# Kernel tuning notes

Measured on AMD Instinct MI355X. Metric: run time of the kernel, lower is better.

Reference implementation:

```python
import jax, jax.numpy as jnp
import numpy as np

B, CIN, T = 16, 1024, 2000
BN, OUT, K = 512, 512, 3
DIL = (1, 2, 3)
NBR = len(DIL)
RED = 1
BN_EPS = 1e-5
STD_EPS = 0.01


def setup_inputs() -> dict:
    key = jax.random.key(0)
    ks = jax.random.split(key, 16)
    inp = {
        "x": jax.random.normal(ks[0], (B, CIN, T), dtype=jnp.float32),
        # BatchNorm1d(in_channels) params + running stats (inference mode)
        "bn1_gamma": jax.random.uniform(ks[1], (CIN,), minval=0.5, maxval=1.5),
        "bn1_beta": jax.random.normal(ks[2], (CIN,)) * 0.1,
        "bn1_mean": jax.random.normal(ks[3], (CIN,)) * 0.1,
        "bn1_var": jax.random.uniform(ks[4], (CIN,), minval=0.5, maxval=1.5),
        # linear1: in_channels -> bn_channels, no bias
        "W1": jax.random.normal(ks[5], (BN, CIN)) * (1.0 / np.sqrt(CIN)),
        # BatchNorm1d(bn_channels)
        "bn2_gamma": jax.random.uniform(ks[6], (BN,), minval=0.5, maxval=1.5),
        "bn2_beta": jax.random.normal(ks[7], (BN,)) * 0.1,
        "bn2_mean": jax.random.normal(ks[8], (BN,)) * 0.1,
        "bn2_var": jax.random.uniform(ks[9], (BN,), minval=0.5, maxval=1.5),
        # per-dilation TimeDelay weights [n_branch, OUT, BN, K] (bias=False)
        "conv_w": jax.random.normal(ks[10], (NBR, OUT, BN, K)) * (1.0 / np.sqrt(OUT)),
        # StatsSelect: linear1 (4C -> C//red), linear2 list (C//red -> C)
        "sel_W1": jax.random.normal(ks[11], (OUT // RED, 4 * OUT)) * (1.0 / np.sqrt(4 * OUT)),
        "sel_b1": jax.random.normal(ks[12], (OUT // RED,)) * 0.01,
        "sel_W2": jax.random.normal(ks[13], (NBR, OUT, OUT // RED)) * (1.0 / np.sqrt(OUT // RED)),
        "sel_b2": jax.random.normal(ks[14], (NBR, OUT)) * 0.01,
    }
    return inp


def _bn_relu(x, gamma, beta, mean, var):
    # inference BatchNorm1d over channel dim, then ReLU; x: [B, C, T]
    inv = gamma / jnp.sqrt(var + BN_EPS)
    y = x * inv[None, :, None] + (beta - mean * inv)[None, :, None]
    return jax.nn.relu(y)


def _forward(x, bn1_gamma, bn1_beta, bn1_mean, bn1_var, W1,
             bn2_gamma, bn2_beta, bn2_mean, bn2_var,
             conv_w, sel_W1, sel_b1, sel_W2, sel_b2):
    # bn_function: nonlinear1 -> linear1 (pointwise over channels)
    h = _bn_relu(x, bn1_gamma, bn1_beta, bn1_mean, bn1_var)  # [B, CIN, T]
    h = jnp.einsum('bct,oc->bot', h, W1)                      # [B, BN, T]
    h = _bn_relu(h, bn2_gamma, bn2_beta, bn2_mean, bn2_var)
    # multi-dilation TDNN branches (dilated conv1d with 'same' padding)
    pad = (K - 1) // 2
    outs = []
    for i, d in enumerate(DIL):
        y = jax.lax.conv_general_dilated(
            h, conv_w[i], window_strides=(1,), padding=[(pad * d, pad * d)],
            rhs_dilation=(d,), dimension_numbers=('NCH', 'OIH', 'NCH'))
        outs.append(y)
    f = jnp.stack(outs, axis=1)  # [B, n, OUT, T]
    xs = jnp.sum(f, axis=1)      # [B, OUT, T]
    # high-order statistics pooling over time
    mean = jnp.mean(xs, axis=-1)                     # [B, OUT]
    std = jnp.std(xs, axis=-1, ddof=1)               # unbiased
    norm = (xs - mean[..., None]) / jnp.clip(std, STD_EPS)[..., None]
    skew = jnp.mean(norm ** 3, axis=-1)
    kurt = jnp.mean(norm ** 4, axis=-1)
    stats = jnp.concatenate([mean, std, skew, kurt], axis=-1)  # [B, 4*OUT]
    z = stats @ sel_W1.T + sel_b1                               # [B, OUT//RED]
    s = jnp.einsum('br,ncr->bnc', z, sel_W2) + sel_b2[None]     # [B, n, OUT]
    s = jax.nn.softmax(s, axis=1)[..., None]                    # [B, n, OUT, 1]
    return jnp.sum(f * s, axis=1)                               # [B, OUT, T]


def reference(x, bn1_gamma, bn1_beta, bn1_mean, bn1_var, W1,
              bn2_gamma, bn2_beta, bn2_mean, bn2_var,
              conv_w, sel_W1, sel_b1, sel_W2, sel_b2):
    return _forward(x, bn1_gamma, bn1_beta, bn1_mean, bn1_var, W1,
                    bn2_gamma, bn2_beta, bn2_mean, bn2_var,
                    conv_w, sel_W1, sel_b1, sel_W2, sel_b2)
```

## Files before the change

kernel.cpp:

```cpp
#include <hip/hip_runtime.h>
#include <hip/hip_bf16.h>

#define B_    16
#define CIN_  1024
#define T_    2000
#define BN_   512
#define OUT_  512
#define NBR_  3
#define TP_X  2048
#define TP_H  2064
#define HOFF  4

typedef float  f32x4  __attribute__((ext_vector_type(4)));
typedef __bf16 bf16x8 __attribute__((ext_vector_type(8)));
typedef unsigned short u16;
typedef u16 u16x4 __attribute__((ext_vector_type(4)));
typedef u16 u16x8 __attribute__((ext_vector_type(8)));

static __device__ __forceinline__ float b2f(u16 u) {
    union { float f; unsigned int i; } v; v.i = ((unsigned int)u) << 16; return v.f;
}
static __device__ __forceinline__ u16 f2b(float f) {
    __hip_bfloat16 h = __float2bfloat16(f);
    u16 r; __builtin_memcpy(&r, &h, 2); return r;
}
static __device__ __forceinline__ void gld16(const u16* g, u16* l) {
    __builtin_amdgcn_global_load_lds(
        (const __attribute__((address_space(1))) unsigned int*)g,
        (__attribute__((address_space(3))) unsigned int*)l, 16, 0, 0);
}

__global__ __launch_bounds__(256) void k_prep_x(
    const float* __restrict__ x, const float* __restrict__ g,
    const float* __restrict__ be, const float* __restrict__ mu,
    const float* __restrict__ va, u16* __restrict__ xbT)
{
    __shared__ float tile[32][33];
    int b = blockIdx.z, c0 = blockIdx.y * 32, t0 = blockIdx.x * 32;
    int tid = threadIdx.x;
    int cl = tid >> 3, tt = (tid & 7) * 4;
    int c = c0 + cl;
    float inv = g[c] / sqrtf(va[c] + 1e-5f);
    float bia = be[c] - mu[c] * inv;
    int t = t0 + tt;
    float y0 = 0.f, y1 = 0.f, y2 = 0.f, y3 = 0.f;
    if (t < T_) {
        float4 v = *reinterpret_cast<const float4*>(x + (size_t)(b * CIN_ + c) * T_ + t);
        y0 = fmaxf(v.x * inv + bia, 0.f);
        y1 = fmaxf(v.y * inv + bia, 0.f);
        y2 = fmaxf(v.z * inv + bia, 0.f);
        y3 = fmaxf(v.w * inv + bia, 0.f);
    }
    tile[tt + 0][cl] = y0; tile[tt + 1][cl] = y1;
    tile[tt + 2][cl] = y2; tile[tt + 3][cl] = y3;
    __syncthreads();
    int tl = tid >> 3, c8 = (tid & 7) * 4;
    u16x4 o;
    o.x = f2b(tile[tl][c8 + 0]);
    o.y = f2b(tile[tl][c8 + 1]);
    o.z = f2b(tile[tl][c8 + 2]);
    o.w = f2b(tile[tl][c8 + 3]);
    *reinterpret_cast<u16x4*>(xbT + (size_t)(b * TP_X + t0 + tl) * CIN_ + c0 + c8) = o;
}

__global__ __launch_bounds__(256) void k_prep_w1(
    const float* __restrict__ W1, const float* __restrict__ g,
    const float* __restrict__ be, const float* __restrict__ mu,
    const float* __restrict__ va, u16* __restrict__ W1b, float* __restrict__ bias2)
{
    int i = blockIdx.x * 256 + threadIdx.x;
    int o = i >> 8;
    int c = (i & 255) * 4;
    float inv = g[o] / sqrtf(va[o] + 1e-5f);
    if (c == 0) bias2[o] = be[o] - mu[o] * inv;
    float4 w = *reinterpret_cast<const float4*>(W1 + (size_t)o * CIN_ + c);
    u16x4 r;
    r.x = f2b(w.x * inv); r.y = f2b(w.y * inv);
    r.z = f2b(w.z * inv); r.w = f2b(w.w * inv);
    *reinterpret_cast<u16x4*>(W1b + (size_t)o * CIN_ + c) = r;
}

__global__ __launch_bounds__(256) void k_prep_wc(
    const float* __restrict__ cw, u16* __restrict__ wb)
{
    int i = blockIdx.x * 256 + threadIdx.x;
    if (i >= NBR_ * OUT_ * BN_) return;
    const float* p = cw + (size_t)i * 3;
    int c = i & 511;
    int o = (i >> 9) & 511;
    int n = i >> 18;
#pragma unroll
    for (int k = 0; k < 3; k++)
        wb[((size_t)(n * 3 + k) * OUT_ + o) * BN_ + c] = f2b(p[k]);
}

__global__ __launch_bounds__(256) void k_zero_hpad(u16* __restrict__ hT)
{
    int i = blockIdx.x * 256 + threadIdx.x;
    if (i >= B_ * 64 * BN_) return;
    int c = i & 511;
    int p = (i >> 9) % 64;
    int b = i / (64 * 512);
    int idx = (p < HOFF) ? p : (p + 2000);
    hT[(size_t)(b * TP_H + idx) * BN_ + c] = 0;
}

__global__ __launch_bounds__(256) void k_gemm1(
    const u16* __restrict__ W1b, const u16* __restrict__ xbT,
    const float* __restrict__ bias2, u16* __restrict__ hT)
{
    __shared__ u16 As[128 * 32];
    __shared__ u16 Bs[128 * 32];
    int tid = threadIdx.x;
    int t0 = blockIdx.x * 128;
    int o0 = blockIdx.y * 128;
    int b  = blockIdx.z;
    int lane = tid & 63, wv = tid >> 6;
    int m_off = (wv & 1) * 64, n_off = (wv >> 1) * 64;
    int lr = lane & 15, g = lane >> 4;

    int s0 = wv * 128 + lane, s1 = s0 + 64;
    size_t ga0 = (size_t)(s0 >> 2) * CIN_ + (((s0 & 3) ^ ((s0 >> 3) & 3)) * 8);
    size_t ga1 = (size_t)(s1 >> 2) * CIN_ + (((s1 & 3) ^ ((s1 >> 3) & 3)) * 8);
    u16* lA0 = As + (size_t)(wv * 128) * 8; u16* lA1 = lA0 + 512;
    u16* lB0 = Bs + (size_t)(wv * 128) * 8; u16* lB1 = lB0 + 512;

    int sw = (g ^ ((lr >> 1) & 3)) * 8;
    int fA[4], fB[4];
#pragma unroll
    for (int m = 0; m < 4; m++) fA[m] = (m_off + m * 16 + lr) * 32 + sw;
#pragma unroll
    for (int n = 0; n < 4; n++) fB[n] = (n_off + n * 16 + lr) * 32 + sw;

    f32x4 zz = {0.f, 0.f, 0.f, 0.f};
    f32x4 acc[4][4];
#pragma unroll
    for (int m = 0; m < 4; m++)
#pragma unroll
        for (int n = 0; n < 4; n++) acc[m][n] = zz;

    const u16* Ag = W1b + (size_t)o0 * CIN_;
    const u16* Bg = xbT + (size_t)(b * TP_X + t0) * CIN_;

    for (int kc = 0; kc < CIN_; kc += 32) {
        gld16(Ag + ga0 + kc, lA0);
        gld16(Ag + ga1 + kc, lA1);
        gld16(Bg + ga0 + kc, lB0);
        gld16(Bg + ga1 + kc, lB1);
        __syncthreads();
        bf16x8 af[4], bfr[4];
#pragma unroll
        for (int m = 0; m < 4; m++) af[m] = *reinterpret_cast<const bf16x8*>(As + fA[m]);
#pragma unroll
        for (int n = 0; n < 4; n++) bfr[n] = *reinterpret_cast<const bf16x8*>(Bs + fB[n]);
#pragma unroll
        for (int m = 0; m < 4; m++)
#pragma unroll
            for (int n = 0; n < 4; n++)
                acc[m][n] = __builtin_amdgcn_mfma_f32_16x16x32_bf16(af[m], bfr[n], acc[m][n], 0, 0, 0);
        __syncthreads();
    }

    int qr = (lane >> 4) * 4;
#pragma unroll
    for (int m = 0; m < 4; m++) {
        int o = o0 + m_off + m * 16 + qr;
        f32x4 bb = *reinterpret_cast<const f32x4*>(bias2 + o);
#pragma unroll
        for (int n = 0; n < 4; n++) {
            int t = t0 + n_off + n * 16 + lr;
            if (t < T_) {
                f32x4 v = acc[m][n];
                u16x4 r;
                r.x = f2b(fmaxf(v.x + bb.x, 0.f));
                r.y = f2b(fmaxf(v.y + bb.y, 0.f));
                r.z = f2b(fmaxf(v.z + bb.z, 0.f));
                r.w = f2b(fmaxf(v.w + bb.w, 0.f));
                *reinterpret_cast<u16x4*>(hT + (size_t)(b * TP_H + t + HOFF) * BN_ + o) = r;
            }
        }
    }
}

__global__ __launch_bounds__(256) void k_conv(
    const u16* __restrict__ hT, const u16* __restrict__ wb, u16* __restrict__ f)
{
    __shared__ u16 As[576 * 8];
    __shared__ u16 Bs[3 * 512 * 8];
    int tid = threadIdx.x;
    int t0 = blockIdx.x * 128;
    int o0 = blockIdx.y * 128;
    int nb = blockIdx.z;
    int n = nb >> 4, b = nb & 15;
    int d = n + 1;
    int lane = tid & 63, wv = tid >> 6;
    int m_off = (wv & 1) * 64, n_off = (wv >> 1) * 64;
    int lr = lane & 15, g = lane >> 4;

    int q1 = tid + 256;
    size_t off0 = (size_t)(tid >> 2) * BN_ + (((tid & 3) ^ ((tid >> 3) & 3)) * 8);
    size_t off1 = (size_t)(q1 >> 2) * BN_ + (((q1 & 3) ^ ((q1 >> 3) & 3)) * 8);
    int q2 = 512 + (lane & 31);
    size_t off2 = (size_t)(q2 >> 2) * BN_ + (((q2 & 3) ^ ((q2 >> 3) & 3)) * 8);
    u16* lA0 = As + (size_t)(wv * 64) * 8;
    u16* lA1 = As + (size_t)(256 + wv * 64) * 8;
    u16* lA2 = As + (size_t)512 * 8;
    u16* lB0 = Bs + (size_t)(wv * 64) * 8;
    u16* lB1 = Bs + (size_t)(256 + wv * 64) * 8;

    int sw = (g ^ ((lr >> 1) & 3)) * 8;
    int fB[4];
#pragma unroll
    for (int nn = 0; nn < 4; nn++) fB[nn] = (n_off + nn * 16 + lr) * 32 + sw;

    f32x4 zz = {0.f, 0.f, 0.f, 0.f};
    f32x4 acc[4][4];
#pragma unroll
    for (int m = 0; m < 4; m++)
#pragma unroll
        for (int nn = 0; nn < 4; nn++) acc[m][nn] = zz;

    const u16* Agh = hT + (size_t)(b * TP_H + t0 - d + HOFF) * BN_;
    const u16* Bg[3];
#pragma unroll
    for (int tap = 0; tap < 3; tap++)
        Bg[tap] = wb + (size_t)((n * 3 + tap) * OUT_ + o0) * BN_;

    for (int kc = 0; kc < BN_; kc += 32) {
        gld16(Agh + off0 + kc, lA0);
        gld16(Agh + off1 + kc, lA1);
        if (wv == 0) gld16(Agh + off2 + kc, lA2);
#pragma unroll
        for (int tap = 0; tap < 3; tap++) {
            gld16(Bg[tap] + off0 + kc, lB0 + tap * 4096);
            gld16(Bg[tap] + off1 + kc, lB1 + tap * 4096);
        }
        __syncthreads();
#pragma unroll
        for (int tap = 0; tap < 3; tap++) {
            int rsh = d * tap;
            bf16x8 af[4], bfr[4];
#pragma unroll
            for (int m = 0; m < 4; m++) {
                int row = m_off + m * 16 + lr + rsh;
                af[m] = *reinterpret_cast<const bf16x8*>(
                    As + row * 32 + ((g ^ ((row >> 1) & 3)) * 8));
            }
#pragma unroll
            for (int nn = 0; nn < 4; nn++)
                bfr[nn] = *reinterpret_cast<const bf16x8*>(Bs + tap * 4096 + fB[nn]);
#pragma unroll
            for (int m = 0; m < 4; m++)
#pragma unroll
                for (int nn = 0; nn < 4; nn++)
                    acc[m][nn] = __builtin_amdgcn_mfma_f32_16x16x32_bf16(af[m], bfr[nn], acc[m][nn], 0, 0, 0);
        }
        __syncthreads();
    }

    int qr = (lane >> 4) * 4;
#pragma unroll
    for (int m = 0; m < 4; m++) {
        int t = t0 + m_off + m * 16 + qr;
#pragma unroll
        for (int nn = 0; nn < 4; nn++) {
            int o = o0 + n_off + nn * 16 + lr;
            f32x4 v = acc[m][nn];
            u16* dst = f + ((size_t)(n * B_ + b) * OUT_ + o) * T_ + t;
            if (t + 3 < T_) {
                u16x4 r;
                r.x = f2b(v.x); r.y = f2b(v.y); r.z = f2b(v.z); r.w = f2b(v.w);
                *reinterpret_cast<u16x4*>(dst) = r;
            } else {
                if (t + 0 < T_) dst[0] = f2b(v.x);
                if (t + 1 < T_) dst[1] = f2b(v.y);
                if (t + 2 < T_) dst[2] = f2b(v.z);
                if (t + 3 < T_) dst[3] = f2b(v.w);
            }
        }
    }
}

__global__ __launch_bounds__(256) void k_stats(
    const u16* __restrict__ f, float* __restrict__ stats)
{
    int bo = blockIdx.x;
    int tid = threadIdx.x;
    const size_t stride = (size_t)B_ * OUT_ * T_;
    double s1 = 0, s2 = 0, s3 = 0, s4 = 0;
    if (tid < 250) {
        const u16* p0 = f + (size_t)bo * T_ + tid * 8;
        u16x8 a0 = *reinterpret_cast<const u16x8*>(p0);
        u16x8 a1 = *reinterpret_cast<const u16x8*>(p0 + stride);
        u16x8 a2 = *reinterpret_cast<const u16x8*>(p0 + 2 * stride);
#pragma unroll
        for (int j = 0; j < 8; j++) {
            float v = b2f(a0[j]) + b2f(a1[j]) + b2f(a2[j]);
            double dd = (double)v, d2 = dd * dd;
            s1 += dd; s2 += d2; s3 += d2 * dd; s4 += d2 * d2;
        }
    }
    for (int off = 32; off > 0; off >>= 1) {
        s1 += __shfl_down(s1, off);
        s2 += __shfl_down(s2, off);
        s3 += __shfl_down(s3, off);
        s4 += __shfl_down(s4, off);
    }
    __shared__ double red[4][4];
    int lane = tid & 63, wv = tid >> 6;
    if (lane == 0) { red[wv][0] = s1; red[wv][1] = s2; red[wv][2] = s3; red[wv][3] = s4; }
    __syncthreads();
    if (tid == 0) {
        double a1 = 0, a2 = 0, a3 = 0, a4 = 0;
        for (int w = 0; w < 4; w++) { a1 += red[w][0]; a2 += red[w][1]; a3 += red[w][2]; a4 += red[w][3]; }
        const double Tn = (double)T_;
        double m1 = a1 / Tn, m2 = a2 / Tn, m3 = a3 / Tn, m4 = a4 / Tn;
        double c2 = m2 - m1 * m1; if (c2 < 0) c2 = 0;
        double stdv = sqrt(c2 * (Tn / (Tn - 1.0)));
        double sc = stdv > 0.01 ? stdv : 0.01;
        double c3 = m3 - 3.0 * m1 * m2 + 2.0 * m1 * m1 * m1;
        double c4 = m4 - 4.0 * m1 * m3 + 6.0 * m1 * m1 * m2 - 3.0 * m1 * m1 * m1 * m1;
        int b = bo >> 9, o = bo & 511;
        float* sp = stats + (size_t)b * 2048;
        sp[o]        = (float)m1;
        sp[512 + o]  = (float)stdv;
        sp[1024 + o] = (float)(c3 / (sc * sc * sc));
        sp[1536 + o] = (float)(c4 / (sc * sc * sc * sc));
    }
}

__global__ __launch_bounds__(256) void k_sel1(
    const float* __restrict__ stats, const float* __restrict__ W1s,
    const float* __restrict__ b1s, float* __restrict__ z)
{
    int gid = blockIdx.x * 4 + (threadIdx.x >> 6);
    int lane = threadIdx.x & 63;
    int b = gid >> 9, r = gid & 511;
    const float4* wp = reinterpret_cast<const float4*>(W1s + (size_t)r * 2048 + lane * 32);
    const float4* sp = reinterpret_cast<const float4*>(stats + (size_t)b * 2048 + lane * 32);
    float acc = 0.f;
#pragma unroll
    for (int j = 0; j < 8; j++) {
        float4 w = wp[j], s = sp[j];
        acc += w.x * s.x + w.y * s.y + w.z * s.z + w.w * s.w;
    }
#pragma unroll
    for (int off = 32; off > 0; off >>= 1) acc += __shfl_down(acc, off);
    if (lane == 0) z[gid] = acc + b1s[r];
}

__global__ __launch_bounds__(256) void k_sel2(
    const float* __restrict__ z, const float* __restrict__ W2s,
    const float* __restrict__ b2s, float* __restrict__ s)
{
    int gid = blockIdx.x * 4 + (threadIdx.x >> 6);
    int lane = threadIdx.x & 63;
    int b = gid >> 9, c = gid & 511;
    const float4* zp = reinterpret_cast<const float4*>(z + (size_t)b * 512 + lane * 8);
    float4 z0 = zp[0], z1 = zp[1];
    float a[3];
#pragma unroll
    for (int n = 0; n < 3; n++) {
        const float4* wp = reinterpret_cast<const float4*>(W2s + (size_t)(n * 512 + c) * 512 + lane * 8);
        float4 w0 = wp[0], w1 = wp[1];
        float acc = z0.x * w0.x + z0.y * w0.y + z0.z * w0.z + z0.w * w0.w
                  + z1.x * w1.x + z1.y * w1.y + z1.z * w1.z + z1.w * w1.w;
#pragma unroll
        for (int off = 32; off > 0; off >>= 1) acc += __shfl_down(acc, off);
        a[n] = acc + b2s[n * 512 + c];
    }
    if (lane == 0) {
        float mx = fmaxf(a[0], fmaxf(a[1], a[2]));
        float e0 = expf(a[0] - mx), e1 = expf(a[1] - mx), e2 = expf(a[2] - mx);
        float inv = 1.f / (e0 + e1 + e2);
        s[(b * 3 + 0) * 512 + c] = e0 * inv;
        s[(b * 3 + 1) * 512 + c] = e1 * inv;
        s[(b * 3 + 2) * 512 + c] = e2 * inv;
    }
}

__global__ __launch_bounds__(256) void k_final(
    const u16* __restrict__ f, const float* __restrict__ s, float* __restrict__ out)
{
    int id = blockIdx.x * 256 + threadIdx.x;
    int row = id / 250;
    int t = (id % 250) * 8;
    int b = row >> 9, o = row & 511;
    const size_t stride = (size_t)B_ * OUT_ * T_;
    size_t base = (size_t)row * T_ + t;
    float s0 = s[(b * 3 + 0) * 512 + o];
    float s1 = s[(b * 3 + 1) * 512 + o];
    float s2 = s[(b * 3 + 2) * 512 + o];
    u16x8 a0 = *reinterpret_cast<const u16x8*>(f + base);
    u16x8 a1 = *reinterpret_cast<const u16x8*>(f + stride + base);
    u16x8 a2 = *reinterpret_cast<const u16x8*>(f + 2 * stride + base);
    float4 r0, r1;
    r0.x = s0 * b2f(a0[0]) + s1 * b2f(a1[0]) + s2 * b2f(a2[0]);
    r0.y = s0 * b2f(a0[1]) + s1 * b2f(a1[1]) + s2 * b2f(a2[1]);
    r0.z = s0 * b2f(a0[2]) + s1 * b2f(a1[2]) + s2 * b2f(a2[2]);
    r0.w = s0 * b2f(a0[3]) + s1 * b2f(a1[3]) + s2 * b2f(a2[3]);
    r1.x = s0 * b2f(a0[4]) + s1 * b2f(a1[4]) + s2 * b2f(a2[4]);
    r1.y = s0 * b2f(a0[5]) + s1 * b2f(a1[5]) + s2 * b2f(a2[5]);
    r1.z = s0 * b2f(a0[6]) + s1 * b2f(a1[6]) + s2 * b2f(a2[6]);
    r1.w = s0 * b2f(a0[7]) + s1 * b2f(a1[7]) + s2 * b2f(a2[7]);
    *reinterpret_cast<float4*>(out + base)     = r0;
    *reinterpret_cast<float4*>(out + base + 4) = r1;
}

extern "C" void kernel_launch(void* const* d_in, const int* in_sizes, int n_in,
                              void* d_out, int out_size, void* d_ws, size_t ws_size,
                              hipStream_t stream)
{
    const float* x     = (const float*)d_in[0];
    const float* bn1g  = (const float*)d_in[1];
    const float* bn1b  = (const float*)d_in[2];
    const float* bn1m  = (const float*)d_in[3];
    const float* bn1v  = (const float*)d_in[4];
    const float* W1    = (const float*)d_in[5];
    const float* bn2g  = (const float*)d_in[6];
    const float* bn2b  = (const float*)d_in[7];
    const float* bn2m  = (const float*)d_in[8];
    const float* bn2v  = (const float*)d_in[9];
    const float* convw = (const float*)d_in[10];
    const float* selW1 = (const float*)d_in[11];
    const float* selb1 = (const float*)d_in[12];
    const float* selW2 = (const float*)d_in[13];
    const float* selb2 = (const float*)d_in[14];
    float* out = (float*)d_out;

    char* ws = (char*)d_ws;
    u16*   fbuf  = (u16*)(ws);
    u16*   xbT   = (u16*)(ws);
    u16*   hT    = (u16*)(ws + 98304000);
    u16*   W1b   = (u16*)(ws + 132120576);
    float* bias2 = (float*)(ws + 133169152);
    u16*   wb    = (u16*)(ws + 133171200);
    float* stats = (float*)(ws + 137889792);
    float* zbuf  = (float*)(ws + 138020864);
    float* sbuf  = (float*)(ws + 138053632);

    k_prep_x  <<<dim3(64, 32, 16), 256, 0, stream>>>(x, bn1g, bn1b, bn1m, bn1v, xbT);
    k_prep_w1 <<<512,  256, 0, stream>>>(W1, bn2g, bn2b, bn2m, bn2v, W1b, bias2);
    k_prep_wc <<<3072, 256, 0, stream>>>(convw, wb);
    k_zero_hpad<<<2048, 256, 0, stream>>>(hT);
    k_gemm1   <<<dim3(16, 4, 16), 256, 0, stream>>>(W1b, xbT, bias2, hT);
    k_conv    <<<dim3(16, 4, 48), 256, 0, stream>>>(hT, wb, fbuf);
    k_stats   <<<8192, 256, 0, stream>>>(fbuf, stats);
    k_sel1    <<<2048, 256, 0, stream>>>(stats, selW1, selb1, zbuf);
    k_sel2    <<<2048, 256, 0, stream>>>(zbuf, selW2, selb2, sbuf);
    k_final   <<<8000, 256, 0, stream>>>(fbuf, sbuf, out);
}
```

Before: 504.7 us.

## Double-buffer LDS in GEMM and conv kernels, shrink conv tile, widen prep_x

Both the pointwise GEMM and the dilated conv kernels now ping-pong between two LDS buffers. The next K-chunk's global-to-LDS loads are issued before the MFMAs run on the current chunk, so load latency can hide behind compute. The conv output tile is halved from 128 to 64 channels, which doubles its grid and cuts per-block LDS and accumulator usage. The prep_x transpose now handles 64 channels per block with 8-wide bf16 stores and skips padded time rows. The cost is more LDS per block, possibly lower occupancy, and redundant reloads of the conv input tile across the extra blocks.

```diff
diff --git a/kernel.cpp b/kernel.cpp
--- a/kernel.cpp
+++ b/kernel.cpp
@@ -35,32 +35,32 @@
     const float* __restrict__ be, const float* __restrict__ mu,
     const float* __restrict__ va, u16* __restrict__ xbT)
 {
-    __shared__ float tile[32][33];
-    int b = blockIdx.z, c0 = blockIdx.y * 32, t0 = blockIdx.x * 32;
+    __shared__ float tile[32][65];
+    int b = blockIdx.z, c0 = blockIdx.y * 64, t0 = blockIdx.x * 32;
     int tid = threadIdx.x;
-    int cl = tid >> 3, tt = (tid & 7) * 4;
+    int cl = tid >> 2, sg = (tid & 3) * 4;
     int c = c0 + cl;
     float inv = g[c] / sqrtf(va[c] + 1e-5f);
     float bia = be[c] - mu[c] * inv;
-    int t = t0 + tt;
-    float y0 = 0.f, y1 = 0.f, y2 = 0.f, y3 = 0.f;
-    if (t < T_) {
-        float4 v = *reinterpret_cast<const float4*>(x + (size_t)(b * CIN_ + c) * T_ + t);
-        y0 = fmaxf(v.x * inv + bia, 0.f);
-        y1 = fmaxf(v.y * inv + bia, 0.f);
-        y2 = fmaxf(v.z * inv + bia, 0.f);
-        y3 = fmaxf(v.w * inv + bia, 0.f);
-    }
-    tile[tt + 0][cl] = y0; tile[tt + 1][cl] = y1;
-    tile[tt + 2][cl] = y2; tile[tt + 3][cl] = y3;
+    const float* xp = x + (size_t)(b * CIN_ + c) * T_ + t0;
+#pragma unroll
+    for (int h = 0; h < 2; h++) {
+        int tt = sg + h * 16;
+        float4 v = {0.f, 0.f, 0.f, 0.f};
+        if (t0 + tt < T_) v = *reinterpret_cast<const float4*>(xp + tt);
+        tile[tt + 0][cl] = fmaxf(v.x * inv + bia, 0.f);
+        tile[tt + 1][cl] = fmaxf(v.y * inv + bia, 0.f);
+        tile[tt + 2][cl] = fmaxf(v.z * inv + bia, 0.f);
+        tile[tt + 3][cl] = fmaxf(v.w * inv + bia, 0.f);
+    }
     __syncthreads();
-    int tl = tid >> 3, c8 = (tid & 7) * 4;
-    u16x4 o;
-    o.x = f2b(tile[tl][c8 + 0]);
-    o.y = f2b(tile[tl][c8 + 1]);
-    o.z = f2b(tile[tl][c8 + 2]);
-    o.w = f2b(tile[tl][c8 + 3]);
-    *reinterpret_cast<u16x4*>(xbT + (size_t)(b * TP_X + t0 + tl) * CIN_ + c0 + c8) = o;
+    int tl = tid >> 3, c8 = (tid & 7) * 8;
+    if (t0 + tl < T_) {
+        u16x8 o;
+#pragma unroll
+        for (int j = 0; j < 8; j++) o[j] = f2b(tile[tl][c8 + j]);
+        *reinterpret_cast<u16x8*>(xbT + (size_t)(b * TP_X + t0 + tl) * CIN_ + c0 + c8) = o;
+    }
 }
 
 __global__ __launch_bounds__(256) void k_prep_w1(
@@ -109,8 +109,8 @@
     const u16* __restrict__ W1b, const u16* __restrict__ xbT,
     const float* __restrict__ bias2, u16* __restrict__ hT)
 {
-    __shared__ u16 As[128 * 32];
-    __shared__ u16 Bs[128 * 32];
+    __shared__ u16 As0[128 * 32], As1[128 * 32];
+    __shared__ u16 Bs0[128 * 32], Bs1[128 * 32];
     int tid = threadIdx.x;
     int t0 = blockIdx.x * 128;
     int o0 = blockIdx.y * 128;
@@ -122,8 +122,6 @@
     int s0 = wv * 128 + lane, s1 = s0 + 64;
     size_t ga0 = (size_t)(s0 >> 2) * CIN_ + (((s0 & 3) ^ ((s0 >> 3) & 3)) * 8);
     size_t ga1 = (size_t)(s1 >> 2) * CIN_ + (((s1 & 3) ^ ((s1 >> 3) & 3)) * 8);
-    u16* lA0 = As + (size_t)(wv * 128) * 8; u16* lA1 = lA0 + 512;
-    u16* lB0 = Bs + (size_t)(wv * 128) * 8; u16* lB1 = lB0 + 512;
 
     int sw = (g ^ ((lr >> 1) & 3)) * 8;
     int fA[4], fB[4];
@@ -142,23 +140,33 @@
     const u16* Ag = W1b + (size_t)o0 * CIN_;
     const u16* Bg = xbT + (size_t)(b * TP_X + t0) * CIN_;
 
-    for (int kc = 0; kc < CIN_; kc += 32) {
-        gld16(Ag + ga0 + kc, lA0);
-        gld16(Ag + ga1 + kc, lA1);
-        gld16(Bg + ga0 + kc, lB0);
-        gld16(Bg + ga1 + kc, lB1);
-        __syncthreads();
+    auto stage = [&](u16* A, u16* Bb, int kc) {
+        gld16(Ag + ga0 + kc, A + wv * 1024);
+        gld16(Ag + ga1 + kc, A + wv * 1024 + 512);
+        gld16(Bg + ga0 + kc, Bb + wv * 1024);
+        gld16(Bg + ga1 + kc, Bb + wv * 1024 + 512);
+    };
+    auto compute = [&](const u16* A, const u16* Bb) {
         bf16x8 af[4], bfr[4];
 #pragma unroll
-        for (int m = 0; m < 4; m++) af[m] = *reinterpret_cast<const bf16x8*>(As + fA[m]);
-#pragma unroll
-        for (int n = 0; n < 4; n++) bfr[n] = *reinterpret_cast<const bf16x8*>(Bs + fB[n]);
+        for (int m = 0; m < 4; m++) af[m] = *reinterpret_cast<const bf16x8*>(A + fA[m]);
+#pragma unroll
+        for (int n = 0; n < 4; n++) bfr[n] = *reinterpret_cast<const bf16x8*>(Bb + fB[n]);
 #pragma unroll
         for (int m = 0; m < 4; m++)
 #pragma unroll
             for (int n = 0; n < 4; n++)
                 acc[m][n] = __builtin_amdgcn_mfma_f32_16x16x32_bf16(af[m], bfr[n], acc[m][n], 0, 0, 0);
+    };
+
+    stage(As0, Bs0, 0);
+    for (int it = 0; it < 16; it++) {
         __syncthreads();
+        stage(As1, Bs1, it * 64 + 32);
+        compute(As0, Bs0);
+        __syncthreads();
+        if (it < 15) stage(As0, Bs0, it * 64 + 64);
+        compute(As1, Bs1);
     }
 
     int qr = (lane >> 4) * 4;
@@ -185,77 +193,82 @@
 __global__ __launch_bounds__(256) void k_conv(
     const u16* __restrict__ hT, const u16* __restrict__ wb, u16* __restrict__ f)
 {
-    __shared__ u16 As[576 * 8];
-    __shared__ u16 Bs[3 * 512 * 8];
+    __shared__ u16 As0[576 * 8], As1[576 * 8];
+    __shared__ u16 Bs0[768 * 8], Bs1[768 * 8];
     int tid = threadIdx.x;
     int t0 = blockIdx.x * 128;
-    int o0 = blockIdx.y * 128;
+    int o0 = blockIdx.y * 64;
     int nb = blockIdx.z;
     int n = nb >> 4, b = nb & 15;
     int d = n + 1;
     int lane = tid & 63, wv = tid >> 6;
-    int m_off = (wv & 1) * 64, n_off = (wv >> 1) * 64;
+    int m_off = (wv & 1) * 64, n_off = (wv >> 1) * 32;
     int lr = lane & 15, g = lane >> 4;
 
+    size_t offA0 = (size_t)(tid >> 2) * BN_ + (((tid & 3) ^ ((tid >> 3) & 3)) * 8);
     int q1 = tid + 256;
-    size_t off0 = (size_t)(tid >> 2) * BN_ + (((tid & 3) ^ ((tid >> 3) & 3)) * 8);
-    size_t off1 = (size_t)(q1 >> 2) * BN_ + (((q1 & 3) ^ ((q1 >> 3) & 3)) * 8);
+    size_t offA1 = (size_t)(q1 >> 2) * BN_ + (((q1 & 3) ^ ((q1 >> 3) & 3)) * 8);
     int q2 = 512 + (lane & 31);
-    size_t off2 = (size_t)(q2 >> 2) * BN_ + (((q2 & 3) ^ ((q2 >> 3) & 3)) * 8);
-    u16* lA0 = As + (size_t)(wv * 64) * 8;
-    u16* lA1 = As + (size_t)(256 + wv * 64) * 8;
-    u16* lA2 = As + (size_t)512 * 8;
-    u16* lB0 = Bs + (size_t)(wv * 64) * 8;
-    u16* lB1 = Bs + (size_t)(256 + wv * 64) * 8;
+    size_t offA2 = (size_t)(q2 >> 2) * BN_ + (((q2 & 3) ^ ((q2 >> 3) & 3)) * 8);
+    auto boff = [&](int q) -> size_t {
+        int ra = q >> 2, tap = ra >> 6, row = ra & 63;
+        return ((size_t)(n * 3 + tap) * OUT_ + o0 + row) * BN_ +
+               (((q & 3) ^ ((q >> 3) & 3)) * 8);
+    };
+    size_t offB0 = boff(tid), offB1 = boff(tid + 256), offB2 = boff(tid + 512);
 
     int sw = (g ^ ((lr >> 1) & 3)) * 8;
-    int fB[4];
-#pragma unroll
-    for (int nn = 0; nn < 4; nn++) fB[nn] = (n_off + nn * 16 + lr) * 32 + sw;
+    int fB[2];
+#pragma unroll
+    for (int nn = 0; nn < 2; nn++) fB[nn] = (n_off + nn * 16 + lr) * 32 + sw;
 
     f32x4 zz = {0.f, 0.f, 0.f, 0.f};
-    f32x4 acc[4][4];
+    f32x4 acc[4][2];
 #pragma unroll
     for (int m = 0; m < 4; m++)
 #pragma unroll
-        for (int nn = 0; nn < 4; nn++) acc[m][nn] = zz;
+        for (int nn = 0; nn < 2; nn++) acc[m][nn] = zz;
 
     const u16* Agh = hT + (size_t)(b * TP_H + t0 - d + HOFF) * BN_;
-    const u16* Bg[3];
-#pragma unroll
-    for (int tap = 0; tap < 3; tap++)
-        Bg[tap] = wb + (size_t)((n * 3 + tap) * OUT_ + o0) * BN_;
-
-    for (int kc = 0; kc < BN_; kc += 32) {
-        gld16(Agh + off0 + kc, lA0);
-        gld16(Agh + off1 + kc, lA1);
-        if (wv == 0) gld16(Agh + off2 + kc, lA2);
-#pragma unroll
-        for (int tap = 0; tap < 3; tap++) {
-            gld16(Bg[tap] + off0 + kc, lB0 + tap * 4096);
-            gld16(Bg[tap] + off1 + kc, lB1 + tap * 4096);
-        }
-        __syncthreads();
+
+    auto stage = [&](u16* A, u16* Bb, int kc) {
+        gld16(Agh + offA0 + kc, A + wv * 512);
+        gld16(Agh + offA1 + kc, A + 2048 + wv * 512);
+        if (wv == 0) gld16(Agh + offA2 + kc, A + 4096);
+        gld16(wb + offB0 + kc, Bb + wv * 512);
+        gld16(wb + offB1 + kc, Bb + 2048 + wv * 512);
+        gld16(wb + offB2 + kc, Bb + 4096 + wv * 512);
+    };
+    auto compute = [&](const u16* A, const u16* Bb) {
 #pragma unroll
         for (int tap = 0; tap < 3; tap++) {
             int rsh = d * tap;
-            bf16x8 af[4], bfr[4];
+            bf16x8 af[4], bfr[2];
 #pragma unroll
             for (int m = 0; m < 4; m++) {
                 int row = m_off + m * 16 + lr + rsh;
                 af[m] = *reinterpret_cast<const bf16x8*>(
-                    As + row * 32 + ((g ^ ((row >> 1) & 3)) * 8));
+                    A + row * 32 + ((g ^ ((row >> 1) & 3)) * 8));
             }
 #pragma unroll
-            for (int nn = 0; nn < 4; nn++)
-                bfr[nn] = *reinterpret_cast<const bf16x8*>(Bs + tap * 4096 + fB[nn]);
+            for (int nn = 0; nn < 2; nn++)
+                bfr[nn] = *reinterpret_cast<const bf16x8*>(Bb + tap * 2048 + fB[nn]);
 #pragma unroll
             for (int m = 0; m < 4; m++)
 #pragma unroll
-                for (int nn = 0; nn < 4; nn++)
+                for (int nn = 0; nn < 2; nn++)
                     acc[m][nn] = __builtin_amdgcn_mfma_f32_16x16x32_bf16(af[m], bfr[nn], acc[m][nn], 0, 0, 0);
         }
+    };
+
+    stage(As0, Bs0, 0);
+    for (int it = 0; it < 8; it++) {
         __syncthreads();
+        stage(As1, Bs1, it * 64 + 32);
+        compute(As0, Bs0);
+        __syncthreads();
+        if (it < 7) stage(As0, Bs0, it * 64 + 64);
+        compute(As1, Bs1);
     }
 
     int qr = (lane >> 4) * 4;
@@ -263,7 +276,7 @@
     for (int m = 0; m < 4; m++) {
         int t = t0 + m_off + m * 16 + qr;
 #pragma unroll
-        for (int nn = 0; nn < 4; nn++) {
+        for (int nn = 0; nn < 2; nn++) {
             int o = o0 + n_off + nn * 16 + lr;
             f32x4 v = acc[m][nn];
             u16* dst = f + ((size_t)(n * B_ + b) * OUT_ + o) * T_ + t;
@@ -439,12 +452,12 @@
     float* zbuf  = (float*)(ws + 138020864);
     float* sbuf  = (float*)(ws + 138053632);
 
-    k_prep_x  <<<dim3(64, 32, 16), 256, 0, stream>>>(x, bn1g, bn1b, bn1m, bn1v, xbT);
+    k_prep_x  <<<dim3(63, 16, 16), 256, 0, stream>>>(x, bn1g, bn1b, bn1m, bn1v, xbT);
     k_prep_w1 <<<512,  256, 0, stream>>>(W1, bn2g, bn2b, bn2m, bn2v, W1b, bias2);
     k_prep_wc <<<3072, 256, 0, stream>>>(convw, wb);
     k_zero_hpad<<<2048, 256, 0, stream>>>(hT);
     k_gemm1   <<<dim3(16, 4, 16), 256, 0, stream>>>(W1b, xbT, bias2, hT);
-    k_conv    <<<dim3(16, 4, 48), 256, 0, stream>>>(hT, wb, fbuf);
+    k_conv    <<<dim3(16, 8, 48), 256, 0, stream>>>(hT, wb, fbuf);
     k_stats   <<<8192, 256, 0, stream>>>(fbuf, stats);
     k_sel1    <<<2048, 256, 0, stream>>>(stats, selW1, selb1, zbuf);
     k_sel2    <<<2048, 256, 0, stream>>>(zbuf, selW2, selb2, sbuf);
```

Measured after the change: 530.6 us. 5.1% more time.
